# Performance work log

Measured on AMD Instinct MI355X. Metric: run time of the kernel, lower is better.

Reference implementation:

```python
import jax, jax.numpy as jnp
import numpy as np
from jax import lax

K = 3
ITERATIONS = 100
LR = 0.01
UMIN, UMAX = 0.0, 63.0
MOMENTUM = 0.7
SQRT2 = float(np.sqrt(2.0))
NDC = float(0.5 * np.log(2.0 * np.pi))  # log-normalizing constant of N(0,1)


def _gausshermite(k):
    x, w = np.polynomial.hermite.hermgauss(k)
    sh = (1, 1, 1, 1, -1)
    xn = x.reshape(sh)
    wn = (w / np.sqrt(np.pi)).reshape(sh)
    xi = np.repeat(x, k).reshape(sh)   # pairwise grid, k^2 points
    xj = np.tile(x, k).reshape(sh)
    we = (np.outer(w, w) / np.pi).reshape(sh)
    f = lambda a: jnp.asarray(a, dtype=jnp.float32)
    return f(xn), f(xi), f(xj), f(wn), f(we)

XN, XI, XJ, WN, WE = _gausshermite(K)
X22 = 2 * XN ** 2 - 1
XIJ = XI * XJ
XI2AXJ2 = XI ** 2 + XJ ** 2 - 1
XI2MXJ2 = XI ** 2 - XJ ** 2


def setup_inputs() -> dict:
    key = jax.random.key(0)
    k1, k2, k3 = jax.random.split(key, 3)
    B, H, W = 4, 256, 256
    y = jax.random.uniform(k1, (B, H, W), dtype=jnp.float32) * 63.0
    edge_weight = jax.random.normal(k2, (B, H, W, 2), dtype=jnp.float32) * 0.1
    unary = jax.random.normal(k3, (B, H, W, 2), dtype=jnp.float32) * 0.05
    return {"y": y, "edge_weight": edge_weight, "unary": unary}


def _osi2(y, edge_weight, unary):
    yi = y[..., None, None]             # [B,H,W,1,1]
    ew = edge_weight[..., None]         # [B,H,W,2,1]
    uw1 = unary[..., 0:1][..., None]    # [B,H,W,1,1]
    uw2 = unary[..., 1:2][..., None]
    mu = yi
    sigma = jnp.ones_like(mu)
    rou = ew / (jnp.max(ew) * 1.01 + 1.0)
    v = jnp.zeros(ew.shape[:3] + (4, 1), dtype=ew.dtype)

    def step(carry, _):
        mu, sigma, rou, v = carry
        # unary quadrature: [B,H,W,1,K]
        xn_pts = XN * sigma * SQRT2 + mu
        fn = xn_pts * (uw1 * xn_pts + uw2 * yi)
        fn = (fn - 3 * (NDC + jnp.log(sigma))) * WN
        # pairwise quadrature over right/down neighbors: [B,H,W,2,K^2]
        q = 1 - rou ** 2
        rtq = jnp.sqrt(q)
        s = jnp.sqrt(1 + rou) / 2
        r = jnp.sqrt(1 - rou) / 2
        z1 = (s + r) * XI + (s - r) * XJ
        z2 = (s - r) * XI + (s + r) * XJ
        o2 = jnp.concatenate([jnp.roll(sigma, -1, 1), jnp.roll(sigma, -1, 2)], axis=3)
        mu2 = jnp.concatenate([jnp.roll(mu, -1, 1), jnp.roll(mu, -1, 2)], axis=3)
        fe = ew * (z1 * sigma * SQRT2 + mu) * (z2 * o2 * SQRT2 + mu2)
        fe = (fe + (2 * NDC + jnp.log(sigma * o2) + jnp.log(q) / 2)) * WE
        # natural-gradient updates
        dmu = jnp.sum(fn * XN, -1, keepdims=True) / sigma * SQRT2
        dmu += jnp.sum(jnp.sum(fe * (z1 - rou * z2), -1, keepdims=True) / (sigma * q) * SQRT2, 3, keepdims=True)
        dmu2 = jnp.sum(fe * (z2 - rou * z1), -1, keepdims=True) / (o2 * q) * SQRT2
        dmu += jnp.roll(dmu2[..., 0:1, :], 1, 1) + jnp.roll(dmu2[..., 1:2, :], 1, 2)
        dsigma = jnp.sum(fn * X22, -1, keepdims=True) / sigma
        dsigma += jnp.sum(jnp.sum(fe * (XI2AXJ2 + XI2MXJ2 / rtq), -1, keepdims=True) / sigma, 3, keepdims=True)
        dsigma2 = jnp.sum(fe * (XI2AXJ2 - XI2MXJ2 / rtq), -1, keepdims=True) / o2
        dsigma += jnp.roll(dsigma2[..., 0:1, :], 1, 1) + jnp.roll(dsigma2[..., 1:2, :], 1, 2)
        drou = jnp.sum(fe * (2 * XIJ - rou * XI2AXJ2), -1, keepdims=True) / q
        # momentum state update with clipping
        v = MOMENTUM * v + LR * jnp.concatenate([dmu, dsigma, drou], axis=3)
        mu = jnp.clip(mu + v[..., 0:1, :], UMIN, UMAX)
        sigma = jnp.clip(sigma + v[..., 1:2, :], 0.001, 50.0)
        rou = jnp.clip(rou + v[..., 2:4, :], -0.99, 0.99)
        return (mu, sigma, rou, v), None

    (mu, sigma, rou, v), _ = lax.scan(jax.checkpoint(step), (mu, sigma, rou, v), None, length=ITERATIONS)
    return mu[..., 0, 0]


def reference(y, edge_weight, unary):
    return _osi2(y, edge_weight, unary)
```

## Files before the change

### kernel.cpp

```cpp
#include <hip/hip_runtime.h>
#include <math.h>

#define NPIX  262144
#define NEDGE 524288
#define T     10
#define TILE_R 54
#define TILE_C 52
#define TS     53
#define RPT    3
#define NRG    18
#define ACTIVE (TILE_C*NRG)
#define NTHR   1024
#define HALO_R 11
#define HALO_C 10

__device__ __forceinline__ float clampf(float x, float lo, float hi) {
    return fminf(fmaxf(x, lo), hi);
}

__global__ __launch_bounds__(NTHR) void tile_kernel(
    const float* __restrict__ muI, const float* __restrict__ vI,
    float* __restrict__ muO, float* __restrict__ vO,
    const float4* __restrict__ c1,
    float* __restrict__ mu_out,
    int first)
{
    __shared__ float buf[2][TILE_R*TS];

    int tid = threadIdx.x;
    int rg  = tid / TILE_C;
    int col = tid - rg*TILE_C;
    bool act = (tid < ACTIVE);
    int bz = blockIdx.z;
    int h0 = blockIdx.y * 32;
    int w0 = blockIdx.x * 32;
    int w  = (w0 + col - HALO_C) & 255;
    int r0 = RPT*rg;

    float mu[RPT], v[RPT];
    float4 k1[RPT];
    float k2x0;
    float k2y[RPT];
    int hh[RPT];

    if (act) {
#pragma unroll
        for (int k = 0; k < RPT; ++k) {
            int r = r0 + k;
            int h = (h0 + r - HALO_R) & 255;
            hh[k] = h;
            int g = (bz << 16) | (h << 8) | w;
            float m = muI[g];
            mu[k] = m;
            buf[0][r*TS + col] = m;
            k1[k] = c1[g];
            v[k] = first ? 0.f : vI[g];
        }
        int hu = (h0 + ((r0 == 0) ? 0 : r0-1) - HALO_R) & 255;
        k2x0 = c1[(bz << 16) | (hu << 8) | w].z;
        int wl = (w0 + ((col == 0) ? 0 : col-1) - HALO_C) & 255;
#pragma unroll
        for (int k = 0; k < RPT; ++k)
            k2y[k] = c1[(bz << 16) | (hh[k] << 8) | wl].w;
    }
    __syncthreads();

    int cl = (col == 0)        ? 0        : col-1;
    int cr = (col == TILE_C-1) ? TILE_C-1 : col+1;
    for (int s = 0; s < T; ++s) {
        const float* __restrict__ cur = buf[s & 1];
        float*       __restrict__ nxt = buf[(s & 1) ^ 1];
        int rgLo = (s + 2) / 3;
        int rgHi = (51 - s) / 3;
        if (act && rg >= rgLo && rg <= rgHi) {
            float nmu[RPT];
            float up0 = cur[((rg == 0)     ? 0          : (r0-1))*TS + col];
            float dnL = cur[((rg == NRG-1) ? (TILE_R-1) : (r0+RPT))*TS + col];
#pragma unroll
            for (int k = 0; k < RPT; ++k) {
                int r = r0 + k;
                float lf = cur[r*TS + cl];
                float rt = cur[r*TS + cr];
                float up = (k == 0)     ? up0 : mu[k-1];
                float dn = (k == RPT-1) ? dnL : mu[k+1];
                float4 K = k1[k];
                float K2x = (k == 0) ? k2x0 : k1[k-1].z;
                float dmu = K.x*mu[k] + K.y + K.z*dn + K.w*rt
                          + K2x*up + k2y[k]*lf;
                v[k] = 0.7f*v[k] + 0.01f*dmu;
                nmu[k] = clampf(mu[k] + v[k], 0.f, 63.f);
            }
#pragma unroll
            for (int k = 0; k < RPT; ++k) {
                mu[k] = nmu[k];
                nxt[(r0 + k)*TS + col] = nmu[k];
            }
        }
        __syncthreads();
    }

    if (act && col >= HALO_C && col < HALO_C+32) {
#pragma unroll
        for (int k = 0; k < RPT; ++k) {
            int r = r0 + k;
            if (r >= HALO_R && r < HALO_R+32) {
                int g = (bz << 16) | (hh[k] << 8) | w;
                if (mu_out) {
                    mu_out[g] = mu[k];
                } else {
                    muO[g] = mu[k];
                    vO[g]  = v[k];
                }
            }
        }
    }
}

__global__ void reduce_max_kernel(const float* __restrict__ ew, unsigned int* gmax) {
    int i = blockIdx.x*blockDim.x + threadIdx.x;
    float m = -INFINITY;
    for (; i < NEDGE; i += gridDim.x*blockDim.x) m = fmaxf(m, ew[i]);
#pragma unroll
    for (int off = 32; off > 0; off >>= 1)
        m = fmaxf(m, __shfl_down(m, off, 64));
    if ((threadIdx.x & 63) == 0) {
        unsigned u = __float_as_uint(m);
        unsigned key = (u & 0x80000000u) ? ~u : (u | 0x80000000u);
        atomicMax(gmax, key);
    }
}

__global__ __launch_bounds__(256) void init_state_kernel(
    const float*  __restrict__ y,
    const float2* __restrict__ ew,
    const float2* __restrict__ uw,
    float* muA, float4* c1)
{
    int idx = blockIdx.x*256 + threadIdx.x;
    float2 e   = ew[idx];
    float2 uwv = uw[idx];
    float  yv  = y[idx];
    muA[idx] = yv;
    c1[idx]  = make_float4(2.f*uwv.x, uwv.y*yv, e.x, e.y);
}

extern "C" void kernel_launch(void* const* d_in, const int* in_sizes, int n_in,
                              void* d_out, int out_size, void* d_ws, size_t ws_size,
                              hipStream_t stream) {
    const float* y  = (const float*)d_in[0];
    const float* ew = (const float*)d_in[1];
    const float* uw = (const float*)d_in[2];
    float* out = (float*)d_out;
    const int N = NPIX;

    float4* c1  = (float4*)d_ws;
    float*  muA = (float*)(c1 + N);
    float*  muB = muA + N;
    float*  vA  = muB + N;
    float*  vB  = vA + N;

    hipLaunchKernelGGL(init_state_kernel, dim3(N/256), dim3(256), 0, stream,
                       y, (const float2*)ew, (const float2*)uw, muA, c1);

    float *muI = muA, *muO = muB, *vI = vA, *vO = vB;
    const int NLAUNCH = 100 / T;
    for (int l = 0; l < NLAUNCH; ++l) {
        float* mo = (l == NLAUNCH-1) ? out : nullptr;
        hipLaunchKernelGGL(tile_kernel, dim3(8, 8, 4), dim3(NTHR), 0, stream,
                           muI, vI, muO, vO, c1, mo, (l == 0) ? 1 : 0);
        float* t;
        t = muI; muI = muO; muO = t;
        t = vI;  vI  = vO;  vO  = t;
    }
}
```

Measured before the change: 151.7 us.

## Remap tile threads to 4-column row segments with vectorized LDS access

```diff
diff --git a/kernel.cpp b/kernel.cpp
--- a/kernel.cpp
+++ b/kernel.cpp
@@ -1,16 +1,14 @@
 #include <hip/hip_runtime.h>
 #include <math.h>
 
-#define NPIX  262144
-#define NEDGE 524288
-#define T     10
+#define NPIX   262144
+#define T      10
 #define TILE_R 54
 #define TILE_C 52
-#define TS     53
-#define RPT    3
-#define NRG    18
-#define ACTIVE (TILE_C*NRG)
-#define NTHR   1024
+#define TS     60
+#define NCG    13
+#define ACTIVE (TILE_R*NCG)
+#define NTHR   768
 #define HALO_R 11
 #define HALO_C 10
 
@@ -26,107 +24,91 @@
     int first)
 {
     __shared__ float buf[2][TILE_R*TS];
+    __shared__ float ewz[TILE_R*TS];
+    __shared__ float eww[TILE_R*TS];
 
     int tid = threadIdx.x;
-    int rg  = tid / TILE_C;
-    int col = tid - rg*TILE_C;
+    int r   = tid / NCG;
+    int cg  = tid - r*NCG;
     bool act = (tid < ACTIVE);
     int bz = blockIdx.z;
     int h0 = blockIdx.y * 32;
     int w0 = blockIdx.x * 32;
-    int w  = (w0 + col - HALO_C) & 255;
-    int r0 = RPT*rg;
+    int c0 = 4*cg;
+    int h  = (h0 + r - HALO_R) & 255;
 
-    float mu[RPT], v[RPT];
-    float4 k1[RPT];
-    float k2x0;
-    float k2y[RPT];
-    int hh[RPT];
+    float mu[4], v[4];
+    float4 k1[4];
+    float k2x[4], k2y = 0.f;
+    int gi[4];
 
     if (act) {
 #pragma unroll
-        for (int k = 0; k < RPT; ++k) {
-            int r = r0 + k;
-            int h = (h0 + r - HALO_R) & 255;
-            hh[k] = h;
-            int g = (bz << 16) | (h << 8) | w;
-            float m = muI[g];
-            mu[k] = m;
-            buf[0][r*TS + col] = m;
-            k1[k] = c1[g];
-            v[k] = first ? 0.f : vI[g];
+        for (int j = 0; j < 4; ++j) {
+            int wv = (w0 + c0 + j - HALO_C) & 255;
+            gi[j] = (bz << 16) | (h << 8) | wv;
+            mu[j] = muI[gi[j]];
+            v[j]  = first ? 0.f : vI[gi[j]];
+            float4 K = c1[gi[j]];
+            k1[j] = K;
+            buf[0][r*TS + c0 + j] = mu[j];
+            ewz[r*TS + c0 + j] = K.z;
+            eww[r*TS + c0 + j] = K.w;
         }
-        int hu = (h0 + ((r0 == 0) ? 0 : r0-1) - HALO_R) & 255;
-        k2x0 = c1[(bz << 16) | (hu << 8) | w].z;
-        int wl = (w0 + ((col == 0) ? 0 : col-1) - HALO_C) & 255;
-#pragma unroll
-        for (int k = 0; k < RPT; ++k)
-            k2y[k] = c1[(bz << 16) | (hh[k] << 8) | wl].w;
     }
     __syncthreads();
 
-    int cl = (col == 0)        ? 0        : col-1;
-    int cr = (col == TILE_C-1) ? TILE_C-1 : col+1;
+    if (act) {
+        int ru = (r == 0) ? 0 : r-1;
+        float4 t = *(const float4*)&ewz[ru*TS + c0];
+        k2x[0] = t.x; k2x[1] = t.y; k2x[2] = t.z; k2x[3] = t.w;
+        k2y = eww[r*TS + ((cg == 0) ? 0 : c0-1)];
+    }
+
     for (int s = 0; s < T; ++s) {
         const float* __restrict__ cur = buf[s & 1];
         float*       __restrict__ nxt = buf[(s & 1) ^ 1];
-        int rgLo = (s + 2) / 3;
-        int rgHi = (51 - s) / 3;
-        if (act && rg >= rgLo && rg <= rgHi) {
-            float nmu[RPT];
-            float up0 = cur[((rg == 0)     ? 0          : (r0-1))*TS + col];
-            float dnL = cur[((rg == NRG-1) ? (TILE_R-1) : (r0+RPT))*TS + col];
+        if (act && r >= 2+s && r <= 51-s) {
+            float4 up4 = *(const float4*)&cur[(r-1)*TS + c0];
+            float4 dn4 = *(const float4*)&cur[(r+1)*TS + c0];
+            float lf = cur[r*TS + ((cg == 0)     ? 0  : c0-1)];
+            float rt = cur[r*TS + ((cg == NCG-1) ? 51 : c0+4)];
+            float up[4] = {up4.x, up4.y, up4.z, up4.w};
+            float dn[4] = {dn4.x, dn4.y, dn4.z, dn4.w};
+            float nmu[4];
 #pragma unroll
-            for (int k = 0; k < RPT; ++k) {
-                int r = r0 + k;
-                float lf = cur[r*TS + cl];
-                float rt = cur[r*TS + cr];
-                float up = (k == 0)     ? up0 : mu[k-1];
-                float dn = (k == RPT-1) ? dnL : mu[k+1];
-                float4 K = k1[k];
-                float K2x = (k == 0) ? k2x0 : k1[k-1].z;
-                float dmu = K.x*mu[k] + K.y + K.z*dn + K.w*rt
-                          + K2x*up + k2y[k]*lf;
-                v[k] = 0.7f*v[k] + 0.01f*dmu;
-                nmu[k] = clampf(mu[k] + v[k], 0.f, 63.f);
+            for (int j = 0; j < 4; ++j) {
+                float L = (j == 0) ? lf : mu[j-1];
+                float R = (j == 3) ? rt : mu[j+1];
+                float4 K = k1[j];
+                float K2x = k2x[j];
+                float K2y = (j == 0) ? k2y : k1[j-1].w;
+                float dmu = K.x*mu[j] + K.y + K.z*dn[j] + K.w*R
+                          + K2x*up[j] + K2y*L;
+                v[j] = 0.7f*v[j] + 0.01f*dmu;
+                nmu[j] = clampf(mu[j] + v[j], 0.f, 63.f);
             }
+            float4 o = make_float4(nmu[0], nmu[1], nmu[2], nmu[3]);
+            *(float4*)&nxt[r*TS + c0] = o;
 #pragma unroll
-            for (int k = 0; k < RPT; ++k) {
-                mu[k] = nmu[k];
-                nxt[(r0 + k)*TS + col] = nmu[k];
-            }
+            for (int j = 0; j < 4; ++j) mu[j] = nmu[j];
         }
         __syncthreads();
     }
 
-    if (act && col >= HALO_C && col < HALO_C+32) {
+    if (act && r >= HALO_R && r < HALO_R+32) {
 #pragma unroll
-        for (int k = 0; k < RPT; ++k) {
-            int r = r0 + k;
-            if (r >= HALO_R && r < HALO_R+32) {
-                int g = (bz << 16) | (hh[k] << 8) | w;
+        for (int j = 0; j < 4; ++j) {
+            int c = c0 + j;
+            if (c >= HALO_C && c < HALO_C+32) {
                 if (mu_out) {
-                    mu_out[g] = mu[k];
+                    mu_out[gi[j]] = mu[j];
                 } else {
-                    muO[g] = mu[k];
-                    vO[g]  = v[k];
+                    muO[gi[j]] = mu[j];
+                    vO[gi[j]]  = v[j];
                 }
             }
         }
-    }
-}
-
-__global__ void reduce_max_kernel(const float* __restrict__ ew, unsigned int* gmax) {
-    int i = blockIdx.x*blockDim.x + threadIdx.x;
-    float m = -INFINITY;
-    for (; i < NEDGE; i += gridDim.x*blockDim.x) m = fmaxf(m, ew[i]);
-#pragma unroll
-    for (int off = 32; off > 0; off >>= 1)
-        m = fmaxf(m, __shfl_down(m, off, 64));
-    if ((threadIdx.x & 63) == 0) {
-        unsigned u = __float_as_uint(m);
-        unsigned key = (u & 0x80000000u) ? ~u : (u | 0x80000000u);
-        atomicMax(gmax, key);
     }
 }
 
```

Measured after the change: 163.6 us. 1.08x slower.

## Use 64-wide tiles with DPP lane shifts and deeper temporal blocking

Applied to the files above, without the earlier changes.

```diff
diff --git a/kernel.cpp b/kernel.cpp
--- a/kernel.cpp
+++ b/kernel.cpp
@@ -2,20 +2,25 @@
 #include <math.h>
 
 #define NPIX  262144
-#define NEDGE 524288
-#define T     10
-#define TILE_R 54
-#define TILE_C 52
-#define TS     53
-#define RPT    3
-#define NRG    18
-#define ACTIVE (TILE_C*NRG)
-#define NTHR   1024
-#define HALO_R 11
-#define HALO_C 10
+#define TILE  64
+#define TS    65
+#define RPT   4
+#define NSTRIP 16
+#define NTHR  1024
+#define HALO  16
 
 __device__ __forceinline__ float clampf(float x, float lo, float hi) {
     return fminf(fmaxf(x, lo), hi);
+}
+__device__ __forceinline__ float dpp_shr1(float x) {
+    int i = __builtin_amdgcn_update_dpp(0, __float_as_int(x),
+                                        0x138, 0xf, 0xf, false);
+    return __int_as_float(i);
+}
+__device__ __forceinline__ float dpp_shl1(float x) {
+    int i = __builtin_amdgcn_update_dpp(0, __float_as_int(x),
+                                        0x130, 0xf, 0xf, false);
+    return __int_as_float(i);
 }
 
 __global__ __launch_bounds__(NTHR) void tile_kernel(
@@ -23,66 +28,59 @@
     float* __restrict__ muO, float* __restrict__ vO,
     const float4* __restrict__ c1,
     float* __restrict__ mu_out,
+    int Tl,
     int first)
 {
-    __shared__ float buf[2][TILE_R*TS];
+    __shared__ float buf[2][TILE*TS];
 
-    int tid = threadIdx.x;
-    int rg  = tid / TILE_C;
-    int col = tid - rg*TILE_C;
-    bool act = (tid < ACTIVE);
+    int tid  = threadIdx.x;
+    int rg   = tid >> 6;
+    int lane = tid & 63;
     int bz = blockIdx.z;
     int h0 = blockIdx.y * 32;
     int w0 = blockIdx.x * 32;
-    int w  = (w0 + col - HALO_C) & 255;
+    int w  = (w0 + lane - HALO) & 255;
     int r0 = RPT*rg;
 
     float mu[RPT], v[RPT];
     float4 k1[RPT];
+    float k2y[RPT];
     float k2x0;
-    float k2y[RPT];
-    int hh[RPT];
+    int gi[RPT];
 
-    if (act) {
 #pragma unroll
-        for (int k = 0; k < RPT; ++k) {
-            int r = r0 + k;
-            int h = (h0 + r - HALO_R) & 255;
-            hh[k] = h;
-            int g = (bz << 16) | (h << 8) | w;
-            float m = muI[g];
-            mu[k] = m;
-            buf[0][r*TS + col] = m;
-            k1[k] = c1[g];
-            v[k] = first ? 0.f : vI[g];
-        }
-        int hu = (h0 + ((r0 == 0) ? 0 : r0-1) - HALO_R) & 255;
+    for (int k = 0; k < RPT; ++k) {
+        int h = (h0 + r0 + k - HALO) & 255;
+        gi[k] = (bz << 16) | (h << 8) | w;
+        mu[k] = muI[gi[k]];
+        v[k]  = first ? 0.f : vI[gi[k]];
+        k1[k] = c1[gi[k]];
+        k2y[k] = dpp_shr1(k1[k].w);
+    }
+    {
+        int hu = (h0 + ((rg == 0) ? 0 : r0-1) - HALO) & 255;
         k2x0 = c1[(bz << 16) | (hu << 8) | w].z;
-        int wl = (w0 + ((col == 0) ? 0 : col-1) - HALO_C) & 255;
-#pragma unroll
-        for (int k = 0; k < RPT; ++k)
-            k2y[k] = c1[(bz << 16) | (hh[k] << 8) | wl].w;
     }
+    buf[0][r0*TS + lane]       = mu[0];
+    buf[0][(r0 + 3)*TS + lane] = mu[3];
     __syncthreads();
 
-    int cl = (col == 0)        ? 0        : col-1;
-    int cr = (col == TILE_C-1) ? TILE_C-1 : col+1;
-    for (int s = 0; s < T; ++s) {
+    for (int s = 0; s < Tl; ++s) {
         const float* __restrict__ cur = buf[s & 1];
         float*       __restrict__ nxt = buf[(s & 1) ^ 1];
-        int rgLo = (s + 2) / 3;
-        int rgHi = (51 - s) / 3;
-        if (act && rg >= rgLo && rg <= rgHi) {
+        int lo = 14 - Tl + s;
+        int rgLo = (lo <= 0) ? 0 : ((lo + 3) >> 2);
+        int rgHi = (46 + Tl - s) >> 2;
+        if (rg >= rgLo && rg <= rgHi) {
+            float up0 = cur[((rg == 0)        ? 0        : (r0-1))*TS + lane];
+            float dnL = cur[((rg == NSTRIP-1) ? (TILE-1) : (r0+RPT))*TS + lane];
             float nmu[RPT];
-            float up0 = cur[((rg == 0)     ? 0          : (r0-1))*TS + col];
-            float dnL = cur[((rg == NRG-1) ? (TILE_R-1) : (r0+RPT))*TS + col];
 #pragma unroll
             for (int k = 0; k < RPT; ++k) {
-                int r = r0 + k;
-                float lf = cur[r*TS + cl];
-                float rt = cur[r*TS + cr];
                 float up = (k == 0)     ? up0 : mu[k-1];
                 float dn = (k == RPT-1) ? dnL : mu[k+1];
+                float lf = dpp_shr1(mu[k]);
+                float rt = dpp_shl1(mu[k]);
                 float4 K = k1[k];
                 float K2x = (k == 0) ? k2x0 : k1[k-1].z;
                 float dmu = K.x*mu[k] + K.y + K.z*dn + K.w*rt
@@ -91,42 +89,26 @@
                 nmu[k] = clampf(mu[k] + v[k], 0.f, 63.f);
             }
 #pragma unroll
-            for (int k = 0; k < RPT; ++k) {
-                mu[k] = nmu[k];
-                nxt[(r0 + k)*TS + col] = nmu[k];
-            }
+            for (int k = 0; k < RPT; ++k) mu[k] = nmu[k];
+            nxt[r0*TS + lane]       = mu[0];
+            nxt[(r0 + 3)*TS + lane] = mu[3];
         }
         __syncthreads();
     }
 
-    if (act && col >= HALO_C && col < HALO_C+32) {
+    if (lane >= HALO && lane < HALO+32) {
 #pragma unroll
         for (int k = 0; k < RPT; ++k) {
             int r = r0 + k;
-            if (r >= HALO_R && r < HALO_R+32) {
-                int g = (bz << 16) | (hh[k] << 8) | w;
+            if (r >= HALO && r < HALO+32) {
                 if (mu_out) {
-                    mu_out[g] = mu[k];
+                    mu_out[gi[k]] = mu[k];
                 } else {
-                    muO[g] = mu[k];
-                    vO[g]  = v[k];
+                    muO[gi[k]] = mu[k];
+                    vO[gi[k]]  = v[k];
                 }
             }
         }
-    }
-}
-
-__global__ void reduce_max_kernel(const float* __restrict__ ew, unsigned int* gmax) {
-    int i = blockIdx.x*blockDim.x + threadIdx.x;
-    float m = -INFINITY;
-    for (; i < NEDGE; i += gridDim.x*blockDim.x) m = fmaxf(m, ew[i]);
-#pragma unroll
-    for (int off = 32; off > 0; off >>= 1)
-        m = fmaxf(m, __shfl_down(m, off, 64));
-    if ((threadIdx.x & 63) == 0) {
-        unsigned u = __float_as_uint(m);
-        unsigned key = (u & 0x80000000u) ? ~u : (u | 0x80000000u);
-        atomicMax(gmax, key);
     }
 }
 
@@ -162,12 +144,12 @@
     hipLaunchKernelGGL(init_state_kernel, dim3(N/256), dim3(256), 0, stream,
                        y, (const float2*)ew, (const float2*)uw, muA, c1);
 
+    static const int Tls[7] = {15, 15, 15, 15, 15, 15, 10};
     float *muI = muA, *muO = muB, *vI = vA, *vO = vB;
-    const int NLAUNCH = 100 / T;
-    for (int l = 0; l < NLAUNCH; ++l) {
-        float* mo = (l == NLAUNCH-1) ? out : nullptr;
+    for (int l = 0; l < 7; ++l) {
+        float* mo = (l == 6) ? out : nullptr;
         hipLaunchKernelGGL(tile_kernel, dim3(8, 8, 4), dim3(NTHR), 0, stream,
-                           muI, vI, muO, vO, c1, mo, (l == 0) ? 1 : 0);
+                           muI, vI, muO, vO, c1, mo, Tls[l], (l == 0) ? 1 : 0);
         float* t;
         t = muI; muI = muO; muO = t;
         t = vI;  vI  = vO;  vO  = t;
```

After: 141.1 us. 1.08x faster.
